# Kernel optimization log

Hardware: AMD Instinct MI355X
Metric: run time of the kernel (lower is better)

Reference implementation:

```python
import jax, jax.numpy as jnp
import numpy as np

DIM = 1024
STATE = 16
K = 4
INNER = 2048
BATCH = 4
SEQ = 2048
EPS = 1e-6


def silu(x):
    return x * jax.nn.sigmoid(x)


def setup_inputs() -> dict:
    key = jax.random.key(0)
    ks = jax.random.split(key, 8)
    g = lambda k, s, sc: jax.random.normal(k, s, dtype=jnp.float32) * sc
    return {
        "x": jax.random.normal(ks[0], (BATCH, SEQ, DIM), dtype=jnp.float32),
        "w_norm": jnp.ones((DIM,), jnp.float32),
        "W_in": g(ks[1], (2 * INNER, DIM), 0.02),
        "conv_w": g(ks[2], (INNER, K), 0.2),  # depthwise conv kernel
        "conv_b": jnp.zeros((INNER,), jnp.float32),
        "W_dt": g(ks[3], (INNER, INNER), 0.02),
        "b_dt": jnp.zeros((INNER,), jnp.float32),
        "W_B": g(ks[4], (STATE, INNER), 0.02),
        "W_C": g(ks[5], (STATE, INNER), 0.02),
        "A_log": jnp.log(jnp.broadcast_to(jnp.arange(1, STATE + 1, dtype=jnp.float32), (INNER, STATE))),
        "D": jnp.ones((INNER,), jnp.float32),
        "W_out": g(ks[6], (DIM, INNER), 0.02),
    }


def reference(x, w_norm, W_in, conv_w, conv_b, W_dt, b_dt, W_B, W_C, A_log, D, W_out):
    b, L, d = x.shape
    # RMSNorm
    x_norm = x * jax.lax.rsqrt(jnp.mean(x * x, axis=-1, keepdims=True) + EPS) * w_norm
    # input projection and split
    x_and_res = x_norm @ W_in.T  # (b, L, 2*inner)
    x_inner, res = jnp.split(x_and_res, 2, axis=-1)
    # causal depthwise conv1d (pad left K-1, kernel per channel)
    xp = jnp.pad(x_inner, ((0, 0), (K - 1, 0), (0, 0)))
    x_conv = sum(xp[:, j:j + L, :] * conv_w[:, j] for j in range(K)) + conv_b
    x_conv = silu(x_conv)
    # SSM parameters
    dt = jax.nn.softplus(x_conv @ W_dt.T + b_dt)  # (b, L, inner)
    Bm = x_conv @ W_B.T  # (b, L, state)
    Cm = x_conv @ W_C.T  # (b, L, state)
    A = -jnp.exp(A_log)  # (inner, state)

    def step(h, inp):
        dt_t, B_t, C_t, xc_t = inp  # (b,inner),(b,state),(b,state),(b,inner)
        dA = jnp.exp(A * dt_t[..., None])  # (b, inner, state)
        h = dA * h + (dt_t[..., None] * B_t[:, None, :]) * xc_t[..., None]
        y_t = jnp.einsum('bis,bs->bi', h, C_t) + D * xc_t
        return h, y_t

    h0 = jnp.zeros((b, INNER, STATE), x.dtype)
    xs = (dt.transpose(1, 0, 2), Bm.transpose(1, 0, 2), Cm.transpose(1, 0, 2), x_conv.transpose(1, 0, 2))
    _, y = jax.lax.scan(step, h0, xs)  # y: (L, b, inner)
    y = y.transpose(1, 0, 2)
    y = y * silu(res)
    return y @ W_out.T
```

## Files before the change

### kernel.cpp

```cpp
#include <hip/hip_runtime.h>


typedef __bf16 bf16;
typedef __attribute__((ext_vector_type(8))) __bf16 bf16x8;
typedef __attribute__((ext_vector_type(4))) float f32x4;

#define DIM   1024
#define STATE 16
#define INNER 2048
#define BATCH 4
#define SEQ   2048
#define ROWS  (BATCH * SEQ)
#define N1    (2 * INNER)
#define NBC   2176
#define CHUNK 128
#define NC    (SEQ / CHUNK)
#define PF2   4

#define GLOAD_LDS16(g, l)                                                  \
  __builtin_amdgcn_global_load_lds(                                        \
      (const __attribute__((address_space(1))) unsigned int*)(g),          \
      (__attribute__((address_space(3))) unsigned int*)(l), 16, 0, 0)

__global__ void ws_report_kernel(float* out, float wssz, float need) {
  if (threadIdx.x == 0) { out[0] = wssz; out[1] = need; }
}

__global__ __launch_bounds__(256) void rmsnorm_kernel(
    const float* __restrict__ x, const float* __restrict__ w,
    bf16* __restrict__ out) {
  const int row = blockIdx.x;
  const int t = threadIdx.x;
  const float4 v = ((const float4*)(x + (long)row * DIM))[t];
  float ss = v.x * v.x + v.y * v.y + v.z * v.z + v.w * v.w;
#pragma unroll
  for (int off = 32; off > 0; off >>= 1) ss += __shfl_xor(ss, off, 64);
  __shared__ float red[4];
  if ((t & 63) == 0) red[t >> 6] = ss;
  __syncthreads();
  const float tot = red[0] + red[1] + red[2] + red[3];
  const float scale = rsqrtf(tot * (1.0f / DIM) + 1e-6f);
  const float4 wv = ((const float4*)w)[t];
  bf16* o = out + (long)row * DIM + t * 4;
  o[0] = (bf16)(v.x * scale * wv.x);
  o[1] = (bf16)(v.y * scale * wv.y);
  o[2] = (bf16)(v.z * scale * wv.z);
  o[3] = (bf16)(v.w * scale * wv.w);
}

__global__ __launch_bounds__(256) void cvt_bf16_kernel(
    const float* __restrict__ src, bf16* __restrict__ dst, int n) {
  const int i = blockIdx.x * 256 + threadIdx.x;
  if (i < n) dst[i] = (bf16)src[i];
}

__global__ __launch_bounds__(256) void build_wbc_kernel(
    const float* __restrict__ WB, const float* __restrict__ WC,
    bf16* __restrict__ dst) {
  const int i = blockIdx.x * 256 + threadIdx.x;
  const int r = i >> 11;
  const int k = i & (INNER - 1);
  float v = 0.0f;
  if (r < 16) v = WB[r * INNER + k];
  else if (r < 32) v = WC[(r - 16) * INNER + k];
  dst[i] = (bf16)v;
}

__global__ __launch_bounds__(256) void build_a2_kernel(
    const float* __restrict__ A_log, float* __restrict__ A2) {
  const int i = blockIdx.x * 256 + threadIdx.x;
  A2[i] = -__expf(A_log[i]) * 1.4426950408889634f;
}

template <int EPI, int K, int NX>
__global__ __launch_bounds__(512, 2) void gemm256_kernel(
    const bf16* __restrict__ A, const bf16* __restrict__ B,
    float* __restrict__ Cf, bf16* __restrict__ Cb, bf16* __restrict__ Cb2,
    const float* __restrict__ bias) {
  __shared__ __align__(16) char lds[4][32768];
  const int tid = threadIdx.x;
  const int lane = tid & 63;
  const int wave = tid >> 6;
  const int wm = wave >> 2;
  const int wn = wave & 3;

  const int per = gridDim.x >> 3;
  const int lin = (blockIdx.x & 7) * per + (blockIdx.x >> 3);
  const int row_t = lin / NX;
  const int col_t = lin - row_t * NX;
  const long row0 = (long)row_t * 256;
  const long col0 = (long)col_t * 256;

  const int srow = tid >> 2;
  const int scb = (tid & 3) * 16;
  const int ssw = scb ^ (((srow >> 1) & 3) << 4);
  const char* gA = (const char*)A + (row0 + srow) * (long)(2 * K) + ssw;
  const char* gB = (const char*)B + (col0 + srow) * (long)(2 * K) + ssw;

#define STG_A(bb, r, tt)                                                      \
  GLOAD_LDS16(gA + (long)(r) * 128 * (2 * K) + (long)(tt) * 64,               \
              lds[bb] + (r) * 8192 + srow * 64 + scb)
#define STG_B(bb, r, tt)                                                      \
  GLOAD_LDS16(gB + (long)(r) * 128 * (2 * K) + (long)(tt) * 64,               \
              lds[bb] + 16384 + (r) * 8192 + srow * 64 + scb)

  const int fm = lane & 15;
  const int fq = lane >> 4;
  const int ck = (fq * 16) ^ (((fm >> 1) & 3) << 4);
  const int aro = (wm * 128 + fm) * 64;
  const int bro = (wn * 64 + fm) * 64;

  f32x4 acc[8][4];
#pragma unroll
  for (int i = 0; i < 8; ++i)
#pragma unroll
    for (int n = 0; n < 4; ++n) acc[i][n] = (f32x4){0.f, 0.f, 0.f, 0.f};

  const int NT = K / 32;
#pragma unroll
  for (int t0 = 0; t0 < 3; ++t0) {
    STG_A(t0, 0, t0); STG_A(t0, 1, t0);
    STG_B(t0, 0, t0); STG_B(t0, 1, t0);
  }
  __builtin_amdgcn_sched_barrier(0);
  asm volatile("s_waitcnt vmcnt(8)");
  __builtin_amdgcn_s_barrier();
  __builtin_amdgcn_sched_barrier(0);

#define TILE_STEP(CI)                                                         \
  {                                                                           \
    const bool pf = (t + 3) < NT;                                             \
    bf16x8 al[4], bh[4], ah[4];                                               \
    _Pragma("unroll") for (int i = 0; i < 4; ++i)                             \
        al[i] = *(const bf16x8*)(lds[CI] + aro + i * 1024 + ck);              \
    _Pragma("unroll") for (int n = 0; n < 4; ++n)                             \
        bh[n] = *(const bf16x8*)(lds[CI] + 16384 + bro + n * 1024 + ck);      \
    _Pragma("unroll") for (int i = 0; i < 4; ++i)                             \
        ah[i] = *(const bf16x8*)(lds[CI] + aro + (i + 4) * 1024 + ck);        \
    if (pf) {                                                                 \
      STG_A((CI + 3) & 3, 0, t + 3); STG_A((CI + 3) & 3, 1, t + 3);           \
      STG_B((CI + 3) & 3, 0, t + 3); STG_B((CI + 3) & 3, 1, t + 3);           \
    }                                                                         \
    __builtin_amdgcn_s_setprio(1);                                            \
    _Pragma("unroll") for (int i = 0; i < 4; ++i)                             \
    _Pragma("unroll") for (int n = 0; n < 4; ++n)                             \
        acc[i][n] = __builtin_amdgcn_mfma_f32_16x16x32_bf16(                  \
            al[i], bh[n], acc[i][n], 0, 0, 0);                                \
    _Pragma("unroll") for (int i = 0; i < 4; ++i)                             \
    _Pragma("unroll") for (int n = 0; n < 4; ++n)                             \
        acc[4 + i][n] = __builtin_amdgcn_mfma_f32_16x16x32_bf16(              \
            ah[i], bh[n], acc[4 + i][n], 0, 0, 0);                            \
    __builtin_amdgcn_s_setprio(0);                                            \
    __builtin_amdgcn_sched_barrier(0);     \
    if (t < NT - 3) {                                                         \
      asm volatile("s_waitcnt vmcnt(8)");                                     \
    } else if (t == NT - 3) {                                                 \
      asm volatile("s_waitcnt vmcnt(4)");                                     \
    } else if (t == NT - 2) {                                                 \
      asm volatile("s_waitcnt vmcnt(0)");                                     \
    }                                                                         \
    __builtin_amdgcn_s_barrier();                                             \
    __builtin_amdgcn_sched_barrier(0);               \
    ++t;                                                                      \
  }

  {
    int t = 0;
    for (int tb = 0; tb < NT / 4; ++tb) {
      TILE_STEP(0)
      TILE_STEP(1)
      TILE_STEP(2)
      TILE_STEP(3)
    }
  }
#undef TILE_STEP
#undef STG_A
#undef STG_B

  const int er = fq * 4;
  const long rbase = row0 + wm * 128;
  const long cbase = col0 + wn * 64;
  if (EPI == 0) {
    const long Nn = 256 * NX;
#pragma unroll
    for (int i = 0; i < 8; ++i)
#pragma unroll
      for (int n = 0; n < 4; ++n) {
        const long col = cbase + n * 16 + fm;
        const long rw = rbase + i * 16 + er;
#pragma unroll
        for (int r = 0; r < 4; ++r) Cf[(rw + r) * Nn + col] = acc[i][n][r];
      }
  } else if (EPI == 1) {
#pragma unroll
    for (int i = 0; i < 8; ++i)
#pragma unroll
      for (int n = 0; n < 4; ++n) {
        const long col = cbase + n * 16 + fm;
        const float bs = bias[col];
        const long rw = rbase + i * 16 + er;
#pragma unroll
        for (int r = 0; r < 4; ++r) {
          float z = acc[i][n][r] + bs;
          z = (z > 20.0f) ? z : log1pf(__expf(z));
          Cf[(rw + r) * 2048 + col] = z;
        }
      }
  } else {
    if (col0 < 2048) {
#pragma unroll
      for (int i = 0; i < 8; ++i)
#pragma unroll
        for (int n = 0; n < 4; ++n) {
          const long col = cbase + n * 16 + fm;
          const long rw = rbase + i * 16 + er;
#pragma unroll
          for (int r = 0; r < 4; ++r)
            Cb[(rw + r) * 2048 + col] = (bf16)acc[i][n][r];
        }
    } else {
#pragma unroll
      for (int i = 0; i < 8; ++i)
#pragma unroll
        for (int n = 0; n < 4; ++n) {
          const long col = cbase + n * 16 + fm - 2048;
          const long rw = rbase + i * 16 + er;
#pragma unroll
          for (int r = 0; r < 4; ++r) {
            const float v = acc[i][n][r];
            const float s = v / (1.0f + __expf(-v));
            Cb2[(rw + r) * 2048 + col] = (bf16)s;
          }
        }
    }
  }
}

template <int EPI>
__global__ __launch_bounds__(256) void gemm_bf16_kernel(
    const bf16* __restrict__ A, const bf16* __restrict__ B,
    float* __restrict__ Cf2, int nx, int N, int K) {
  __shared__ __align__(16) bf16 As[128 * 32];
  __shared__ __align__(16) bf16 Bs[128 * 32];
  const int tid = threadIdx.x;
  const int lane = tid & 63;
  const int wave = tid >> 6;

  const int per = gridDim.x >> 3;
  const int lin = (blockIdx.x & 7) * per + (blockIdx.x >> 3);
  const int row_t = lin / nx;
  const int col_t = lin - row_t * nx;
  const long row0 = (long)row_t * 128;
  const long col0 = (long)col_t * 128;

  const int wr = (wave >> 1) * 64;
  const int wc = (wave & 1) * 64;

  f32x4 acc[4][4];
#pragma unroll
  for (int i = 0; i < 4; i++)
#pragma unroll
    for (int j = 0; j < 4; j++) acc[i][j] = (f32x4){0.f, 0.f, 0.f, 0.f};

  const int srow = tid >> 2;
  const int scol = (tid & 3) * 8;
  const bf16* gA0 = A + (row0 + srow) * (long)K + scol;
  const bf16* gA1 = A + (row0 + srow + 64) * (long)K + scol;
  const bf16* gB0 = B + (col0 + srow) * (long)K + scol;
  const bf16* gB1 = B + (col0 + srow + 64) * (long)K + scol;
  bf16* lA0 = As + wave * 512 + lane * 8;
  bf16* lA1 = As + 64 * 32 + wave * 512 + lane * 8;
  bf16* lB0 = Bs + wave * 512 + lane * 8;
  bf16* lB1 = Bs + 64 * 32 + wave * 512 + lane * 8;

  const int fm = lane & 15;
  const int fk = (lane >> 4) * 8;

  for (int k0 = 0; k0 < K; k0 += 32) {
    GLOAD_LDS16(gA0 + k0, lA0);
    GLOAD_LDS16(gA1 + k0, lA1);
    GLOAD_LDS16(gB0 + k0, lB0);
    GLOAD_LDS16(gB1 + k0, lB1);
    __syncthreads();
    bf16x8 af[4], bfv[4];
#pragma unroll
    for (int i = 0; i < 4; i++)
      af[i] = *(const bf16x8*)(As + (wr + i * 16 + fm) * 32 + fk);
#pragma unroll
    for (int j = 0; j < 4; j++)
      bfv[j] = *(const bf16x8*)(Bs + (wc + j * 16 + fm) * 32 + fk);
#pragma unroll
    for (int i = 0; i < 4; i++)
#pragma unroll
      for (int j = 0; j < 4; j++)
        acc[i][j] = __builtin_amdgcn_mfma_f32_16x16x32_bf16(
            af[i], bfv[j], acc[i][j], 0, 0, 0);
    __syncthreads();
  }

  const int er = (lane >> 4) * 4;
  const int ec = lane & 15;
#pragma unroll
  for (int i = 0; i < 4; i++) {
#pragma unroll
    for (int j = 0; j < 4; j++) {
      const long col = col0 + wc + j * 16 + ec;
      const long rw = row0 + wr + i * 16 + er;
#pragma unroll
      for (int r = 0; r < 4; r++) {
        const float v = acc[i][j][r];
        const long row = rw + r;
        if (EPI == 3) {
          if (col < 32) Cf2[row * 32 + col] = v;
        }
      }
    }
  }
}

__global__ __launch_bounds__(256) void conv_silu_kernel(
    const bf16* __restrict__ xin, const float* __restrict__ conv_w,
    const float* __restrict__ conv_b, bf16* __restrict__ xc16) {
  const int c = blockIdx.x * 256 + threadIdx.x;
  const int r = blockIdx.y;
  const int l = r & (SEQ - 1);
  const float4 w = *(const float4*)(conv_w + c * 4);
  float acc = conv_b[c];
#pragma unroll
  for (int j = 0; j < 4; j++) {
    const int lp = l - 3 + j;
    const float xv = (lp >= 0) ? (float)xin[(long)(r - 3 + j) * INNER + c] : 0.0f;
    acc += xv * ((const float*)&w)[j];
  }
  const float s = acc / (1.0f + __expf(-acc));
  xc16[(long)r * INNER + c] = (bf16)s;
}

__global__ __launch_bounds__(256) void scan_pass1_kernel(
    const float* __restrict__ dtm, const float* __restrict__ bc,
    const bf16* __restrict__ xc, const float* __restrict__ A2,
    float* __restrict__ hend, float* __restrict__ dtsum) {
  const int ch = blockIdx.x * 256 + threadIdx.x;
  const int c = blockIdx.y;
  const int b = blockIdx.z;
  const long row0 = (long)b * SEQ + (long)c * CHUNK;

  float a2[16];
#pragma unroll
  for (int q = 0; q < 4; q++) {
    const float4 t = ((const float4*)(A2 + (long)ch * 16))[q];
    a2[q * 4 + 0] = t.x; a2[q * 4 + 1] = t.y;
    a2[q * 4 + 2] = t.z; a2[q * 4 + 3] = t.w;
  }
  float h[16];
#pragma unroll
  for (int s = 0; s < 16; s++) h[s] = 0.0f;
  float dts = 0.0f;

  float dtq[PF2], xcq[PF2];
#pragma unroll
  for (int p = 0; p < PF2; p++) {
    const long r2 = row0 + p;
    dtq[p] = dtm[r2 * INNER + ch];
    xcq[p] = (float)xc[r2 * INNER + ch];
  }
  for (int l0 = 0; l0 <= CHUNK - 2 * PF2; l0 += PF2) {
#pragma unroll
    for (int p = 0; p < PF2; p++) {
      const float dt = dtq[p], xcv = xcq[p];
      const long rp = row0 + l0 + p + PF2;
      dtq[p] = dtm[rp * INNER + ch];
      xcq[p] = (float)xc[rp * INNER + ch];
      const long r = row0 + l0 + p;
      float Bv[16];
#pragma unroll
      for (int k = 0; k < 16; k++) Bv[k] = bc[r * 32 + k];
      dts += dt;
      const float u = dt * xcv;
#pragma unroll
      for (int s = 0; s < 16; s++)
        h[s] = exp2f(a2[s] * dt) * h[s] + Bv[s] * u;
    }
  }
#pragma unroll
  for (int p = 0; p < PF2; p++) {
    const float dt = dtq[p], xcv = xcq[p];
    const long r = row0 + CHUNK - PF2 + p;
    float Bv[16];
#pragma unroll
    for (int k = 0; k < 16; k++) Bv[k] = bc[r * 32 + k];
    dts += dt;
    const float u = dt * xcv;
#pragma unroll
    for (int s = 0; s < 16; s++)
      h[s] = exp2f(a2[s] * dt) * h[s] + Bv[s] * u;
  }

  const long cb = (long)(b * NC + c);
#pragma unroll
  for (int s = 0; s < 16; s++) hend[(cb * 16 + s) * INNER + ch] = h[s];
  dtsum[cb * INNER + ch] = dts;
}

__global__ __launch_bounds__(256) void scan_combine_kernel(
    float* __restrict__ hio, const float* __restrict__ dtsum,
    const float* __restrict__ A2) {
  const int idx = blockIdx.x * 256 + threadIdx.x;
  const int ch = idx & (INNER - 1);
  const int s = (idx >> 11) & 15;
  const int b = idx >> 15;
  const float a2 = A2[(long)ch * 16 + s];
  float H = 0.0f;
  for (int c = 0; c < NC; c++) {
    const long cb = (long)(b * NC + c);
    const long o = (cb * 16 + s) * INNER + ch;
    const float he = hio[o];
    const float ds = dtsum[cb * INNER + ch];
    hio[o] = H;
    H = exp2f(a2 * ds) * H + he;
  }
}

__global__ __launch_bounds__(256) void scan_pass3_kernel(
    const float* __restrict__ dtm, const float* __restrict__ bc,
    const bf16* __restrict__ xc, const bf16* __restrict__ rs,
    const float* __restrict__ A2, const float* __restrict__ Dv,
    const float* __restrict__ hstart, bf16* __restrict__ y) {
  const int ch = blockIdx.x * 256 + threadIdx.x;
  const int c = blockIdx.y;
  const int b = blockIdx.z;
  const long row0 = (long)b * SEQ + (long)c * CHUNK;

  float a2[16];
#pragma unroll
  for (int q = 0; q < 4; q++) {
    const float4 t = ((const float4*)(A2 + (long)ch * 16))[q];
    a2[q * 4 + 0] = t.x; a2[q * 4 + 1] = t.y;
    a2[q * 4 + 2] = t.z; a2[q * 4 + 3] = t.w;
  }
  const float d = Dv[ch];
  const long cb = (long)(b * NC + c);
  float h[16];
#pragma unroll
  for (int s = 0; s < 16; s++) h[s] = hstart[(cb * 16 + s) * INNER + ch];

  float dtq[PF2], xcq[PF2], rsq[PF2];
#pragma unroll
  for (int p = 0; p < PF2; p++) {
    const long r2 = row0 + p;
    dtq[p] = dtm[r2 * INNER + ch];
    xcq[p] = (float)xc[r2 * INNER + ch];
    rsq[p] = (float)rs[r2 * INNER + ch];
  }
  for (int l0 = 0; l0 <= CHUNK - 2 * PF2; l0 += PF2) {
#pragma unroll
    for (int p = 0; p < PF2; p++) {
      const float dt = dtq[p], xcv = xcq[p], rsv = rsq[p];
      const long rp = row0 + l0 + p + PF2;
      dtq[p] = dtm[rp * INNER + ch];
      xcq[p] = (float)xc[rp * INNER + ch];
      rsq[p] = (float)rs[rp * INNER + ch];
      const long r = row0 + l0 + p;
      float Bv[16], Cv[16];
#pragma unroll
      for (int k = 0; k < 16; k++) Bv[k] = bc[r * 32 + k];
#pragma unroll
      for (int k = 0; k < 16; k++) Cv[k] = bc[r * 32 + 16 + k];
      const float u = dt * xcv;
      float yv = d * xcv;
#pragma unroll
      for (int s = 0; s < 16; s++) {
        h[s] = exp2f(a2[s] * dt) * h[s] + Bv[s] * u;
        yv += h[s] * Cv[s];
      }
      y[r * INNER + ch] = (bf16)(yv * rsv);
    }
  }
#pragma unroll
  for (int p = 0; p < PF2; p++) {
    const float dt = dtq[p], xcv = xcq[p], rsv = rsq[p];
    const long r = row0 + CHUNK - PF2 + p;
    float Bv[16], Cv[16];
#pragma unroll
    for (int k = 0; k < 16; k++) Bv[k] = bc[r * 32 + k];
#pragma unroll
    for (int k = 0; k < 16; k++) Cv[k] = bc[r * 32 + 16 + k];
    const float u = dt * xcv;
    float yv = d * xcv;
#pragma unroll
    for (int s = 0; s < 16; s++) {
      h[s] = exp2f(a2[s] * dt) * h[s] + Bv[s] * u;
      yv += h[s] * Cv[s];
    }
    y[r * INNER + ch] = (bf16)(yv * rsv);
  }
}

extern "C" void kernel_launch(void* const* d_in, const int* in_sizes, int n_in,
                              void* d_out, int out_size, void* d_ws,
                              size_t ws_size, hipStream_t stream) {
  (void)in_sizes; (void)n_in; (void)out_size;
  const float* x      = (const float*)d_in[0];
  const float* w_norm = (const float*)d_in[1];
  const float* W_in   = (const float*)d_in[2];
  const float* conv_w = (const float*)d_in[3];
  const float* conv_b = (const float*)d_in[4];
  const float* W_dt   = (const float*)d_in[5];
  const float* b_dt   = (const float*)d_in[6];
  const float* W_B    = (const float*)d_in[7];
  const float* W_C    = (const float*)d_in[8];
  const float* A_log  = (const float*)d_in[9];
  const float* Dv     = (const float*)d_in[10];
  const float* W_out  = (const float*)d_in[11];
  float* out = (float*)d_out;

  const size_t MB = 1024ull * 1024ull;
  char* base = (char*)d_ws;
  bf16*  xnorm  = (bf16*)(base + 0);
  bf16*  win_b  = (bf16*)(base + 16 * MB);
  bf16*  xin_b  = (bf16*)(base + 24 * MB);
  float* dtm    = (float*)(base + 0);
  float* bcm    = (float*)(base + 64 * MB);
  bf16*  res_b  = (bf16*)(base + 65 * MB);
  bf16*  xc_b   = (bf16*)(base + 97 * MB);
  bf16*  wdt_b  = (bf16*)(base + 129 * MB);
  bf16*  wbc_b  = (bf16*)(base + 137 * MB);
  float* hend   = (float*)(base + 129 * MB);
  float* dtsum  = (float*)(base + 137 * MB);
  char*  p2     = base + 129 * MB + (size_t)NBC * INNER * 2;
  bf16*  wout_b = (bf16*)p2;
  float* A2     = (float*)(p2 + (size_t)DIM * INNER * 2);
  bf16*  yb     = (bf16*)(p2 + (size_t)DIM * INNER * 2 +
                          (size_t)INNER * STATE * 4);
  const size_t NEEDED = (size_t)((char*)yb - base) + (size_t)ROWS * INNER * 2;

  if (ws_size < NEEDED) {
    ws_report_kernel<<<1, 64, 0, stream>>>(out, (float)ws_size, (float)NEEDED);
    return;
  }

  rmsnorm_kernel<<<ROWS, 256, 0, stream>>>(x, w_norm, xnorm);

  cvt_bf16_kernel<<<(N1 * DIM) / 256, 256, 0, stream>>>(W_in, win_b, N1 * DIM);
  cvt_bf16_kernel<<<(INNER * INNER) / 256, 256, 0, stream>>>(W_dt, wdt_b,
                                                             INNER * INNER);
  build_wbc_kernel<<<(128 * INNER) / 256, 256, 0, stream>>>(W_B, W_C, wbc_b);
  cvt_bf16_kernel<<<(DIM * INNER) / 256, 256, 0, stream>>>(W_out, wout_b,
                                                           DIM * INNER);
  build_a2_kernel<<<(INNER * STATE) / 256, 256, 0, stream>>>(A_log, A2);

  gemm256_kernel<2, 1024, 16><<<512, 512, 0, stream>>>(
      xnorm, win_b, nullptr, xin_b, res_b, nullptr);

  conv_silu_kernel<<<dim3(INNER / 256, ROWS), 256, 0, stream>>>(
      xin_b, conv_w, conv_b, xc_b);

  gemm256_kernel<1, 2048, 8><<<256, 512, 0, stream>>>(
      xc_b, wdt_b, dtm, nullptr, nullptr, b_dt);

  gemm_bf16_kernel<3><<<64, 256, 0, stream>>>(xc_b, wbc_b, bcm, 1, 128, INNER);

  scan_pass1_kernel<<<dim3(INNER / 256, NC, BATCH), 256, 0, stream>>>(
      dtm, bcm, xc_b, A2, hend, dtsum);
  scan_combine_kernel<<<(BATCH * 16 * INNER) / 256, 256, 0, stream>>>(
      hend, dtsum, A2);
  scan_pass3_kernel<<<dim3(INNER / 256, NC, BATCH), 256, 0, stream>>>(
      dtm, bcm, xc_b, res_b, A2, Dv, hend, yb);

  gemm256_kernel<0, 2048, 4><<<128, 512, 0, stream>>>(
      yb, wout_b, out, nullptr, nullptr, nullptr);
}
```

Baseline: 647.5 us.

## Restructure GEMM to 64-wide K tiles with double buffering and split-K out-projection

The bf16 GEMM kernel changes from four 32-wide K stages to two 64-wide K buffers. Each tile is computed in quarter-sized MFMA groups, with global-to-LDS prefetches for the next tile interleaved between them and barriers placed in between, using a new swizzle. The output projection, which launched only 128 blocks, now uses split-K over 256 blocks writing two partial fp32 results, followed by a separate summation kernel. This is meant to improve latency hiding and occupancy on the small final GEMM, at the cost of extra barriers, extra partial-result traffic and one more launch.

```diff
diff --git a/kernel.cpp b/kernel.cpp
--- a/kernel.cpp
+++ b/kernel.cpp
@@ -72,12 +72,31 @@
   A2[i] = -__expf(A_log[i]) * 1.4426950408889634f;
 }
 
-template <int EPI, int K, int NX>
+__global__ __launch_bounds__(256) void sum2_kernel(
+    const float* __restrict__ p0, const float* __restrict__ p1,
+    float* __restrict__ out) {
+  const long i = (long)blockIdx.x * 256 + threadIdx.x;
+  const float4 a = ((const float4*)p0)[i];
+  const float4 b = ((const float4*)p1)[i];
+  float4 r;
+  r.x = a.x + b.x; r.y = a.y + b.y; r.z = a.z + b.z; r.w = a.w + b.w;
+  ((float4*)out)[i] = r;
+}
+
+#define MFMA_Q(I0, N0)                                                        \
+  _Pragma("unroll") for (int i_ = 0; i_ < 4; ++i_)                            \
+  _Pragma("unroll") for (int n_ = 0; n_ < 2; ++n_)                            \
+  _Pragma("unroll") for (int k_ = 0; k_ < 2; ++k_)                            \
+      acc[(I0) + i_][(N0) + n_] = __builtin_amdgcn_mfma_f32_16x16x32_bf16(    \
+          afr[i_][k_], bfr[(N0) + n_][k_], acc[(I0) + i_][(N0) + n_], 0, 0,   \
+          0);
+
+template <int EPI, int K, int RS, int NX, int KSPLIT>
 __global__ __launch_bounds__(512, 2) void gemm256_kernel(
     const bf16* __restrict__ A, const bf16* __restrict__ B,
     float* __restrict__ Cf, bf16* __restrict__ Cb, bf16* __restrict__ Cb2,
     const float* __restrict__ bias) {
-  __shared__ __align__(16) char lds[4][32768];
+  __shared__ __align__(16) char lds[2][65536];
   const int tid = threadIdx.x;
   const int lane = tid & 63;
   const int wave = tid >> 6;
@@ -85,95 +104,130 @@
   const int wn = wave & 3;
 
   const int per = gridDim.x >> 3;
-  const int lin = (blockIdx.x & 7) * per + (blockIdx.x >> 3);
+  int lin = (blockIdx.x & 7) * per + (blockIdx.x >> 3);
+  int kh = 0;
+  if (KSPLIT) { kh = lin & 1; lin >>= 1; }
   const int row_t = lin / NX;
   const int col_t = lin - row_t * NX;
   const long row0 = (long)row_t * 256;
   const long col0 = (long)col_t * 256;
 
-  const int srow = tid >> 2;
-  const int scb = (tid & 3) * 16;
-  const int ssw = scb ^ (((srow >> 1) & 3) << 4);
-  const char* gA = (const char*)A + (row0 + srow) * (long)(2 * K) + ssw;
-  const char* gB = (const char*)B + (col0 + srow) * (long)(2 * K) + ssw;
-
-#define STG_A(bb, r, tt)                                                      \
-  GLOAD_LDS16(gA + (long)(r) * 128 * (2 * K) + (long)(tt) * 64,               \
-              lds[bb] + (r) * 8192 + srow * 64 + scb)
-#define STG_B(bb, r, tt)                                                      \
-  GLOAD_LDS16(gB + (long)(r) * 128 * (2 * K) + (long)(tt) * 64,               \
-              lds[bb] + 16384 + (r) * 8192 + srow * 64 + scb)
+  const int srow = tid >> 3;
+  const int scb = (tid & 7) * 16;
+  const int ssw = scb ^ ((srow & 7) << 4);
+  const char* gA =
+      (const char*)(A + (size_t)kh * K) + (row0 + srow) * (long)(2 * RS) + ssw;
+  const char* gB =
+      (const char*)(B + (size_t)kh * K) + (col0 + srow) * (long)(2 * RS) + ssw;
+
+#define STG_A(bb, ro, tt)                                                     \
+  GLOAD_LDS16(gA + (long)(ro) * (2 * RS) + (long)(tt) * 128,                  \
+              lds[bb] + ((ro) + srow) * 128 + scb)
+#define STG_B(bb, ro, tt)                                                     \
+  GLOAD_LDS16(gB + (long)(ro) * (2 * RS) + (long)(tt) * 128,                  \
+              lds[bb] + 32768 + ((ro) + srow) * 128 + scb)
 
   const int fm = lane & 15;
   const int fq = lane >> 4;
-  const int ck = (fq * 16) ^ (((fm >> 1) & 3) << 4);
-  const int aro = (wm * 128 + fm) * 64;
-  const int bro = (wn * 64 + fm) * 64;
+  const int swz = (fm & 7) << 4;
+  const int ck0 = (fq * 16) ^ swz;
+  const int ck1 = (64 + fq * 16) ^ swz;
+  const int aro = (wm * 128 + fm) * 128;
+  const int bro = (wn * 64 + fm) * 128;
 
   f32x4 acc[8][4];
 #pragma unroll
   for (int i = 0; i < 8; ++i)
 #pragma unroll
     for (int n = 0; n < 4; ++n) acc[i][n] = (f32x4){0.f, 0.f, 0.f, 0.f};
-
-  const int NT = K / 32;
-#pragma unroll
-  for (int t0 = 0; t0 < 3; ++t0) {
-    STG_A(t0, 0, t0); STG_A(t0, 1, t0);
-    STG_B(t0, 0, t0); STG_B(t0, 1, t0);
-  }
+  bf16x8 afr[4][2], bfr[4][2];
+
+  const int NT = K / 64;
+  STG_B(0, 0, 0);   STG_B(0, 64, 0);
+  STG_B(0, 128, 0); STG_B(0, 192, 0);
+  STG_A(0, 0, 0);   STG_A(0, 128, 0);
+  STG_A(0, 64, 0);  STG_A(0, 192, 0);
   __builtin_amdgcn_sched_barrier(0);
-  asm volatile("s_waitcnt vmcnt(8)");
+  asm volatile("s_waitcnt vmcnt(0)");
   __builtin_amdgcn_s_barrier();
   __builtin_amdgcn_sched_barrier(0);
 
-#define TILE_STEP(CI)                                                         \
+#define TILE64(CI)                                                            \
   {                                                                           \
-    const bool pf = (t + 3) < NT;                                             \
-    bf16x8 al[4], bh[4], ah[4];                                               \
-    _Pragma("unroll") for (int i = 0; i < 4; ++i)                             \
-        al[i] = *(const bf16x8*)(lds[CI] + aro + i * 1024 + ck);              \
-    _Pragma("unroll") for (int n = 0; n < 4; ++n)                             \
-        bh[n] = *(const bf16x8*)(lds[CI] + 16384 + bro + n * 1024 + ck);      \
-    _Pragma("unroll") for (int i = 0; i < 4; ++i)                             \
-        ah[i] = *(const bf16x8*)(lds[CI] + aro + (i + 4) * 1024 + ck);        \
+    const bool pf = (t + 1) < NT;                                             \
+                   \
+    _Pragma("unroll") for (int i_ = 0; i_ < 4; ++i_) {                        \
+      afr[i_][0] = *(const bf16x8*)(lds[CI] + aro + i_ * 2048 + ck0);         \
+      afr[i_][1] = *(const bf16x8*)(lds[CI] + aro + i_ * 2048 + ck1);         \
+    }                                                                         \
+    _Pragma("unroll") for (int n_ = 0; n_ < 2; ++n_) {                        \
+      bfr[n_][0] = *(const bf16x8*)(lds[CI] + 32768 + bro + n_ * 2048 + ck0); \
+      bfr[n_][1] = *(const bf16x8*)(lds[CI] + 32768 + bro + n_ * 2048 + ck1); \
+    }                                                                         \
+    if (pf) { STG_B(CI ^ 1, 0, t + 1); STG_B(CI ^ 1, 64, t + 1); }            \
+    __builtin_amdgcn_s_barrier();                                             \
+    asm volatile("s_waitcnt lgkmcnt(0)");                                     \
+    __builtin_amdgcn_sched_barrier(0);                                        \
+    __builtin_amdgcn_s_setprio(1);                                            \
+    MFMA_Q(0, 0)                                                              \
+    __builtin_amdgcn_s_setprio(0);                                            \
+    __builtin_amdgcn_s_barrier();                                             \
+                  \
+    _Pragma("unroll") for (int n_ = 2; n_ < 4; ++n_) {                        \
+      bfr[n_][0] = *(const bf16x8*)(lds[CI] + 32768 + bro + n_ * 2048 + ck0); \
+      bfr[n_][1] = *(const bf16x8*)(lds[CI] + 32768 + bro + n_ * 2048 + ck1); \
+    }                                                                         \
+    if (pf) { STG_B(CI ^ 1, 128, t + 1); STG_B(CI ^ 1, 192, t + 1); }         \
+    __builtin_amdgcn_s_barrier();                                             \
+    asm volatile("s_waitcnt lgkmcnt(0)");                                     \
+    __builtin_amdgcn_sched_barrier(0);                                        \
+    __builtin_amdgcn_s_setprio(1);                                            \
+    MFMA_Q(0, 2)                                                              \
+    __builtin_amdgcn_s_setprio(0);                                            \
+    __builtin_amdgcn_sched_barrier(0);                                        \
     if (pf) {                                                                 \
-      STG_A((CI + 3) & 3, 0, t + 3); STG_A((CI + 3) & 3, 1, t + 3);           \
-      STG_B((CI + 3) & 3, 0, t + 3); STG_B((CI + 3) & 3, 1, t + 3);           \
-    }                                                                         \
-    __builtin_amdgcn_s_setprio(1);                                            \
-    _Pragma("unroll") for (int i = 0; i < 4; ++i)                             \
-    _Pragma("unroll") for (int n = 0; n < 4; ++n)                             \
-        acc[i][n] = __builtin_amdgcn_mfma_f32_16x16x32_bf16(                  \
-            al[i], bh[n], acc[i][n], 0, 0, 0);                                \
-    _Pragma("unroll") for (int i = 0; i < 4; ++i)                             \
-    _Pragma("unroll") for (int n = 0; n < 4; ++n)                             \
-        acc[4 + i][n] = __builtin_amdgcn_mfma_f32_16x16x32_bf16(              \
-            ah[i], bh[n], acc[4 + i][n], 0, 0, 0);                            \
-    __builtin_amdgcn_s_setprio(0);                                            \
-    __builtin_amdgcn_sched_barrier(0);     \
-    if (t < NT - 3) {                                                         \
-      asm volatile("s_waitcnt vmcnt(8)");                                     \
-    } else if (t == NT - 3) {                                                 \
-      asm volatile("s_waitcnt vmcnt(4)");                                     \
-    } else if (t == NT - 2) {                                                 \
+      asm volatile("s_waitcnt vmcnt(4)");     \
+    } else {                                                                  \
       asm volatile("s_waitcnt vmcnt(0)");                                     \
     }                                                                         \
     __builtin_amdgcn_s_barrier();                                             \
-    __builtin_amdgcn_sched_barrier(0);               \
+    __builtin_amdgcn_sched_barrier(0);                                        \
+                       \
+    _Pragma("unroll") for (int i_ = 0; i_ < 4; ++i_) {                        \
+      afr[i_][0] = *(const bf16x8*)(lds[CI] + aro + (i_ + 4) * 2048 + ck0);   \
+      afr[i_][1] = *(const bf16x8*)(lds[CI] + aro + (i_ + 4) * 2048 + ck1);   \
+    }                                                                         \
+    if (pf) { STG_A(CI ^ 1, 0, t + 1); STG_A(CI ^ 1, 128, t + 1); }           \
+    __builtin_amdgcn_s_barrier();                                             \
+    asm volatile("s_waitcnt lgkmcnt(0)");                                     \
+    __builtin_amdgcn_sched_barrier(0);                                        \
+    __builtin_amdgcn_s_setprio(1);                                            \
+    MFMA_Q(4, 2)                                                              \
+    __builtin_amdgcn_s_setprio(0);                                            \
+    __builtin_amdgcn_s_barrier();                                             \
+          \
+    if (pf) { STG_A(CI ^ 1, 64, t + 1); STG_A(CI ^ 1, 192, t + 1); }          \
+    __builtin_amdgcn_s_barrier();                                             \
+    __builtin_amdgcn_s_setprio(1);                                            \
+    MFMA_Q(4, 0)                                                              \
+    __builtin_amdgcn_s_setprio(0);                                            \
+    __builtin_amdgcn_sched_barrier(0);                                        \
+    if (pf) {                                                                 \
+      asm volatile("s_waitcnt vmcnt(2)");     \
+    }                                                                         \
+    __builtin_amdgcn_s_barrier();                                             \
+    __builtin_amdgcn_sched_barrier(0);                                        \
     ++t;                                                                      \
   }
 
   {
     int t = 0;
-    for (int tb = 0; tb < NT / 4; ++tb) {
-      TILE_STEP(0)
-      TILE_STEP(1)
-      TILE_STEP(2)
-      TILE_STEP(3)
+    for (int tb = 0; tb < NT / 2; ++tb) {
+      TILE64(0)
+      TILE64(1)
     }
   }
-#undef TILE_STEP
+#undef TILE64
 #undef STG_A
 #undef STG_B
 
@@ -182,6 +236,7 @@
   const long cbase = col0 + wn * 64;
   if (EPI == 0) {
     const long Nn = 256 * NX;
+    float* C = Cf + (KSPLIT ? (size_t)kh * ROWS * Nn : 0);
 #pragma unroll
     for (int i = 0; i < 8; ++i)
 #pragma unroll
@@ -189,7 +244,7 @@
         const long col = cbase + n * 16 + fm;
         const long rw = rbase + i * 16 + er;
 #pragma unroll
-        for (int r = 0; r < 4; ++r) Cf[(rw + r) * Nn + col] = acc[i][n][r];
+        for (int r = 0; r < 4; ++r) C[(rw + r) * Nn + col] = acc[i][n][r];
       }
   } else if (EPI == 1) {
 #pragma unroll
@@ -527,6 +582,7 @@
   bf16*  wbc_b  = (bf16*)(base + 137 * MB);
   float* hend   = (float*)(base + 129 * MB);
   float* dtsum  = (float*)(base + 137 * MB);
+  float* gpart  = (float*)(base + 0);
   char*  p2     = base + 129 * MB + (size_t)NBC * INNER * 2;
   bf16*  wout_b = (bf16*)p2;
   float* A2     = (float*)(p2 + (size_t)DIM * INNER * 2);
@@ -549,13 +605,13 @@
                                                            DIM * INNER);
   build_a2_kernel<<<(INNER * STATE) / 256, 256, 0, stream>>>(A_log, A2);
 
-  gemm256_kernel<2, 1024, 16><<<512, 512, 0, stream>>>(
+  gemm256_kernel<2, 1024, 1024, 16, 0><<<512, 512, 0, stream>>>(
       xnorm, win_b, nullptr, xin_b, res_b, nullptr);
 
   conv_silu_kernel<<<dim3(INNER / 256, ROWS), 256, 0, stream>>>(
       xin_b, conv_w, conv_b, xc_b);
 
-  gemm256_kernel<1, 2048, 8><<<256, 512, 0, stream>>>(
+  gemm256_kernel<1, 2048, 2048, 8, 0><<<256, 512, 0, stream>>>(
       xc_b, wdt_b, dtm, nullptr, nullptr, b_dt);
 
   gemm_bf16_kernel<3><<<64, 256, 0, stream>>>(xc_b, wbc_b, bcm, 1, 128, INNER);
@@ -567,6 +623,8 @@
   scan_pass3_kernel<<<dim3(INNER / 256, NC, BATCH), 256, 0, stream>>>(
       dtm, bcm, xc_b, res_b, A2, Dv, hend, yb);
 
-  gemm256_kernel<0, 2048, 4><<<128, 512, 0, stream>>>(
-      yb, wout_b, out, nullptr, nullptr, nullptr);
-}
+  gemm256_kernel<0, 1024, 2048, 4, 1><<<256, 512, 0, stream>>>(
+      yb, wout_b, gpart, nullptr, nullptr, nullptr);
+  sum2_kernel<<<(ROWS * DIM / 4) / 256, 256, 0, stream>>>(
+      gpart, gpart + (size_t)ROWS * DIM, out);
+}
```

Result: no change. 649.7 us (+0.3%).
